# Kernel optimization log

Measured on AMD Instinct MI355X. Metric: run time of the kernel, lower is better.

Reference implementation:

```python
import jax, jax.numpy as jnp
import numpy as np

D_MODEL = 1024
HEADS = 16
D_K = D_MODEL // HEADS


def setup_inputs() -> dict:
    key = jax.random.key(0)
    ks = jax.random.split(key, 11)
    B, S = 4, 2048
    scale = 1.0 / np.sqrt(D_MODEL)
    return {
        "q": jax.random.normal(ks[0], (B, S, D_MODEL), jnp.float32),
        "k": jax.random.normal(ks[1], (B, S, D_MODEL), jnp.float32),
        "v": jax.random.normal(ks[2], (B, S, D_MODEL), jnp.float32),
        "wq": jax.random.normal(ks[3], (D_MODEL, D_MODEL), jnp.float32) * scale,
        "bq": jax.random.normal(ks[4], (D_MODEL,), jnp.float32) * 0.01,
        "wk": jax.random.normal(ks[5], (D_MODEL, D_MODEL), jnp.float32) * scale,
        "bk": jax.random.normal(ks[6], (D_MODEL,), jnp.float32) * 0.01,
        "wv": jax.random.normal(ks[7], (D_MODEL, D_MODEL), jnp.float32) * scale,
        "bv": jax.random.normal(ks[8], (D_MODEL,), jnp.float32) * 0.01,
        "wo": jax.random.normal(ks[9], (D_MODEL, D_MODEL), jnp.float32) * scale,
        "bo": jax.random.normal(ks[10], (D_MODEL,), jnp.float32) * 0.01,
    }


def reference(q, k, v, wq, bq, wk, bk, wv, bv, wo, bo):
    B, S, _ = q.shape
    # nn.Linear: x @ W^T + b
    qp = q @ wq.T + bq
    kp = k @ wk.T + bk
    vp = v @ wv.T + bv
    # [B, S, D] -> [B, H, S, d_k]
    def split_heads(x):
        return x.reshape(B, S, HEADS, D_K).transpose(0, 2, 1, 3)
    qh, kh, vh = split_heads(qp), split_heads(kp), split_heads(vp)
    # scaled dot-product attention (dropout p=0 -> identity)
    scores = jnp.einsum("bhsd,bhtd->bhst", qh, kh) / jnp.sqrt(jnp.float32(D_K)).astype(qh.dtype)
    attn = jax.nn.softmax(scores, axis=-1)
    ctx = jnp.einsum("bhst,bhtd->bhsd", attn, vh)
    # merge heads and output projection
    ctx = ctx.transpose(0, 2, 1, 3).reshape(B, S, D_MODEL)
    return ctx @ wo.T + bo
```

## Files before the change

### kernel.cpp

```cpp
#include <hip/hip_runtime.h>


typedef __attribute__((ext_vector_type(8))) short bf16x8;
typedef __attribute__((ext_vector_type(4))) float f32x4;
typedef unsigned int u32;

#define DEVI __device__ __forceinline__

static constexpr int S_LEN = 2048;
static constexpr int NH = 16;
static constexpr int DK = 64;
static constexpr float Q_SCALE = 0.125f * 1.44269504088896340736f;

DEVI unsigned short f2b(float f) {
    unsigned int u = __builtin_bit_cast(unsigned int, f);
    u += 0x7fffu + ((u >> 16) & 1u);
    return (unsigned short)(u >> 16);
}

DEVI u32 pkbf16(float a, float b) {
#if __has_builtin(__builtin_amdgcn_cvt_pk_bf16_f32)
    auto r = __builtin_amdgcn_cvt_pk_bf16_f32(a, b);
    return __builtin_bit_cast(u32, r);
#else
    return (u32)f2b(a) | ((u32)f2b(b) << 16);
#endif
}

DEVI float fexp2(float x) {
#if __has_builtin(__builtin_amdgcn_exp2f)
    return __builtin_amdgcn_exp2f(x);
#else
    return exp2f(x);
#endif
}

DEVI f32x4 mfma16(bf16x8 a, bf16x8 b, f32x4 c) {
    return __builtin_amdgcn_mfma_f32_16x16x32_bf16(a, b, c, 0, 0, 0);
}

#define GLL16(g, l)                                                        \
    __builtin_amdgcn_global_load_lds(                                      \
        (const __attribute__((address_space(1))) u32*)(g),                 \
        (__attribute__((address_space(3))) u32*)(l), 16, 0, 0)

__global__ __launch_bounds__(256) void cvt3(
    const float* __restrict__ q, const float* __restrict__ k,
    const float* __restrict__ v, unsigned short* __restrict__ dq,
    unsigned short* __restrict__ dk, unsigned short* __restrict__ dv) {
    const int z = blockIdx.y;
    const float* src = z == 0 ? q : z == 1 ? k : v;
    unsigned short* dst = z == 0 ? dq : z == 1 ? dk : dv;
    long i = ((long)blockIdx.x * 256 + threadIdx.x) * 8;
    float4 v0 = *(const float4*)(src + i);
    float4 v1 = *(const float4*)(src + i + 4);
    uint4 o;
    o.x = pkbf16(v0.x, v0.y);
    o.y = pkbf16(v0.z, v0.w);
    o.z = pkbf16(v1.x, v1.y);
    o.w = pkbf16(v1.z, v1.w);
    *(uint4*)(dst + i) = o;
}

__global__ __launch_bounds__(256) void cvt_w(
    const float* __restrict__ a, const float* __restrict__ b,
    const float* __restrict__ c, const float* __restrict__ d,
    unsigned short* __restrict__ o) {
    const float* src = blockIdx.y == 0 ? a : blockIdx.y == 1 ? b
                     : blockIdx.y == 2 ? c : d;
    unsigned short* dst = o + (long)blockIdx.y * 1048576;
    long i = ((long)blockIdx.x * 256 + threadIdx.x) * 8;
    float4 v0 = *(const float4*)(src + i);
    float4 v1 = *(const float4*)(src + i + 4);
    uint4 ov;
    ov.x = pkbf16(v0.x, v0.y);
    ov.y = pkbf16(v0.z, v0.w);
    ov.z = pkbf16(v1.x, v1.y);
    ov.w = pkbf16(v1.z, v1.w);
    *(uint4*)(dst + i) = ov;
}

__global__ __launch_bounds__(256) void gemm_qkv(
    const unsigned short* __restrict__ aq, const unsigned short* __restrict__ ak,
    const unsigned short* __restrict__ av, const unsigned short* __restrict__ wqkv,
    const float* __restrict__ bq, const float* __restrict__ bk,
    const float* __restrict__ bv, unsigned short* __restrict__ qh,
    unsigned short* __restrict__ kh, unsigned short* __restrict__ vht) {
    __shared__ __align__(16) unsigned short As[2][128 * 32];
    __shared__ __align__(16) unsigned short Bs[2][128 * 32];
    const int tid = threadIdx.x;
    const int w = tid >> 6, l = tid & 63, l16 = l & 15, quad = l >> 4;
    const int wm = (w >> 1) * 64, wn = (w & 1) * 64;
    const int m0 = blockIdx.y * 128, n0 = blockIdx.x * 128;
    const int z = blockIdx.z;
    const unsigned short* A = z == 0 ? aq : z == 1 ? ak : av;
    const unsigned short* W = wqkv + (long)z * 1048576;
    const float* bias = z == 0 ? bq : z == 1 ? bk : bv;

    f32x4 acc[4][4] = {};

    auto stage = [&](int kt, int buf) {
        #pragma unroll
        for (int h = 0; h < 2; ++h) {
            int sb = h * 256 + w * 64;
            int slot = sb + l;
            int row = slot >> 2, c = (slot & 3) ^ ((row >> 1) & 3);
            GLL16(A + (long)(m0 + row) * 1024 + kt + c * 8, &As[buf][sb * 8]);
            GLL16(W + (long)(n0 + row) * 1024 + kt + c * 8, &Bs[buf][sb * 8]);
        }
    };

    stage(0, 0);
    __syncthreads();

    for (int ki = 0; ki < 32; ++ki) {
        if (ki < 31) stage((ki + 1) * 32, (ki + 1) & 1);
        const unsigned short* as = As[ki & 1];
        const unsigned short* bs = Bs[ki & 1];
        bf16x8 a[4], b[4];
        #pragma unroll
        for (int i = 0; i < 4; ++i) {
            int r = wm + i * 16 + l16;
            a[i] = *(const bf16x8*)(as + (r * 4 + (quad ^ ((r >> 1) & 3))) * 8);
        }
        #pragma unroll
        for (int j = 0; j < 4; ++j) {
            int r = wn + j * 16 + l16;
            b[j] = *(const bf16x8*)(bs + (r * 4 + (quad ^ ((r >> 1) & 3))) * 8);
        }
        #pragma unroll
        for (int i = 0; i < 4; ++i)
            #pragma unroll
            for (int j = 0; j < 4; ++j)
                acc[i][j] = mfma16(a[i], b[j], acc[i][j]);
        __syncthreads();
    }

    if (z < 2) {
        unsigned short* out = z == 0 ? qh : kh;
        const float scale = z == 0 ? Q_SCALE : 1.0f;
        #pragma unroll
        for (int j = 0; j < 4; ++j) {
            int n = n0 + wn + j * 16 + l16;
            float bvl = bias[n];
            int hh = n >> 6, dd = n & 63;
            #pragma unroll
            for (int i = 0; i < 4; ++i)
                #pragma unroll
                for (int r = 0; r < 4; ++r) {
                    int m = m0 + wm + i * 16 + quad * 4 + r;
                    int bb = m >> 11, ss = m & 2047;
                    out[(((long)(bb * NH + hh) * S_LEN + ss) * DK) + dd] =
                        f2b((acc[i][j][r] + bvl) * scale);
                }
        }
    } else {
        unsigned short* out = vht;
        #pragma unroll
        for (int j = 0; j < 4; ++j) {
            int n = n0 + wn + j * 16 + l16;
            float bvl = bias[n];
            int hh = n >> 6, dd = n & 63;
            #pragma unroll
            for (int i = 0; i < 4; ++i) {
                int m = m0 + wm + i * 16 + quad * 4;
                int bb = m >> 11, ss = m & 2047;
                uint2 pk;
                pk.x = pkbf16(acc[i][j][0] + bvl, acc[i][j][1] + bvl);
                pk.y = pkbf16(acc[i][j][2] + bvl, acc[i][j][3] + bvl);
                *(uint2*)(out + ((long)(bb * NH + hh) * DK + dd) * S_LEN + ss) = pk;
            }
        }
    }
}

__global__ __launch_bounds__(256) void gemm_out(
    const unsigned short* __restrict__ A, const unsigned short* __restrict__ W,
    const float* __restrict__ bias, float* __restrict__ out) {
    __shared__ __align__(16) unsigned short As[2][128 * 32];
    __shared__ __align__(16) unsigned short Bs[2][128 * 32];
    const int tid = threadIdx.x;
    const int w = tid >> 6, l = tid & 63, l16 = l & 15, quad = l >> 4;
    const int wm = (w >> 1) * 64, wn = (w & 1) * 64;
    const int m0 = blockIdx.y * 128, n0 = blockIdx.x * 128;

    f32x4 acc[4][4] = {};

    auto stage = [&](int kt, int buf) {
        #pragma unroll
        for (int h = 0; h < 2; ++h) {
            int sb = h * 256 + w * 64;
            int slot = sb + l;
            int row = slot >> 2, c = (slot & 3) ^ ((row >> 1) & 3);
            GLL16(A + (long)(m0 + row) * 1024 + kt + c * 8, &As[buf][sb * 8]);
            GLL16(W + (long)(n0 + row) * 1024 + kt + c * 8, &Bs[buf][sb * 8]);
        }
    };

    stage(0, 0);
    __syncthreads();

    for (int ki = 0; ki < 32; ++ki) {
        if (ki < 31) stage((ki + 1) * 32, (ki + 1) & 1);
        const unsigned short* as = As[ki & 1];
        const unsigned short* bs = Bs[ki & 1];
        bf16x8 a[4], b[4];
        #pragma unroll
        for (int i = 0; i < 4; ++i) {
            int r = wm + i * 16 + l16;
            a[i] = *(const bf16x8*)(as + (r * 4 + (quad ^ ((r >> 1) & 3))) * 8);
        }
        #pragma unroll
        for (int j = 0; j < 4; ++j) {
            int r = wn + j * 16 + l16;
            b[j] = *(const bf16x8*)(bs + (r * 4 + (quad ^ ((r >> 1) & 3))) * 8);
        }
        #pragma unroll
        for (int i = 0; i < 4; ++i)
            #pragma unroll
            for (int j = 0; j < 4; ++j)
                acc[i][j] = mfma16(a[i], b[j], acc[i][j]);
        __syncthreads();
    }

    #pragma unroll
    for (int j = 0; j < 4; ++j) {
        int n = n0 + wn + j * 16 + l16;
        float bv = bias[n];
        #pragma unroll
        for (int i = 0; i < 4; ++i)
            #pragma unroll
            for (int r = 0; r < 4; ++r) {
                int m = m0 + wm + i * 16 + quad * 4 + r;
                out[(long)m * 1024 + n] = acc[i][j][r] + bv;
            }
    }
}

__global__ __launch_bounds__(256, 3) void attn(
    const unsigned short* __restrict__ qh, const unsigned short* __restrict__ kh,
    const unsigned short* __restrict__ vht, unsigned short* __restrict__ ctx) {
    __shared__ __align__(16) unsigned short Kb[2][4096];
    __shared__ __align__(16) unsigned short Vb[3][4096];
    __shared__ __align__(16) unsigned short P[128 * 44];

    const int id = blockIdx.y * 16 + blockIdx.x;
    const int id2 = (id & 7) * 128 + (id >> 3);
    const int qt = id2 & 15, bh = id2 >> 4;
    const int tid = threadIdx.x;
    const int w = tid >> 6, l = tid & 63, l16 = l & 15, quad = l >> 4;

    const unsigned short* kh_b = kh + (long)bh * 2048 * 64;
    const unsigned short* vh_b = vht + (long)bh * 64 * 2048;

    const unsigned short* qsrc = qh + ((long)bh * 2048 + qt * 128) * 64;
    bf16x8 qf[2][2];
    #pragma unroll
    for (int dd = 0; dd < 2; ++dd)
        #pragma unroll
        for (int i = 0; i < 2; ++i)
            qf[dd][i] = *(const bf16x8*)(qsrc + (w * 32 + i * 16 + l16) * 64 +
                                         dd * 32 + quad * 8);
    #pragma unroll
    for (int dd = 0; dd < 2; ++dd)
        #pragma unroll
        for (int i = 0; i < 2; ++i)
            asm volatile("" :: "v"(qf[dd][i]));

    auto stage_k = [&](const unsigned short* base, int buf) {
        #pragma unroll
        for (int rr = 0; rr < 2; ++rr) {
            int sb = rr * 256 + w * 64;
            int slot = sb + l;
            int row = slot >> 3, cc = (slot & 7) ^ (row & 7);
            GLL16(base + (long)row * 64 + cc * 8, &Kb[buf][sb * 8]);
        }
    };
    auto stage_v = [&](const unsigned short* vbase, int buf) {
        #pragma unroll
        for (int rr = 0; rr < 2; ++rr) {
            int sb = rr * 256 + w * 64;
            int slot = sb + l;
            int d = slot >> 3, cc = (slot & 7) ^ (d & 7);
            GLL16(vbase + (long)d * 2048 + cc * 8, &Vb[buf][sb * 8]);
        }
    };

    stage_k(kh_b, 0);
    stage_v(vh_b, 0);
    stage_v(vh_b + 64, 1);
    asm volatile("s_waitcnt vmcnt(2)" ::: "memory");
    __builtin_amdgcn_s_barrier();
    __builtin_amdgcn_sched_barrier(0);

    f32x4 o[4][2] = {};
    f32x4 osum[2] = {};
    bf16x8 ones;
    #pragma unroll
    for (int j = 0; j < 8; ++j) ones[j] = (short)0x3f80;

    const unsigned short* kstage = kh_b + 64 * 64;
    const unsigned short* vstage = vh_b + 2 * 64;
    int vr = 0, vs = 2;
    for (int kt = 0; kt < 32; ++kt) {
        if (kt < 31) stage_k(kstage, (kt + 1) & 1);
        if (kt < 30) stage_v(vstage, vs);
        kstage += 64 * 64;
        vstage += 64;
        __builtin_amdgcn_sched_barrier(0);

        const unsigned short* kb = Kb[kt & 1];
        f32x4 sa[2][4] = {};
        #pragma unroll
        for (int dd = 0; dd < 2; ++dd) {
            bf16x8 kf[4];
            #pragma unroll
            for (int ja = 0; ja < 4; ++ja) {
                int row = ja * 16 + l16;
                kf[ja] = *(const bf16x8*)(kb + (row * 8 + ((dd * 4 + quad) ^ (row & 7))) * 8);
            }
            __builtin_amdgcn_s_setprio(1);
            #pragma unroll
            for (int i = 0; i < 2; ++i)
                #pragma unroll
                for (int ja = 0; ja < 4; ++ja)
                    sa[i][ja] = mfma16(kf[ja], qf[dd][i], sa[i][ja]);
            __builtin_amdgcn_s_setprio(0);
        }

        #pragma unroll
        for (int i = 0; i < 2; ++i)
            #pragma unroll
            for (int ja = 0; ja < 4; ++ja)
                #pragma unroll
                for (int r = 0; r < 4; ++r)
                    sa[i][ja][r] = fexp2(sa[i][ja][r]);

        const unsigned short* vb = Vb[vr];
        #pragma unroll
        for (int qtr = 0; qtr < 2; ++qtr) {
            #pragma unroll
            for (int jh = 0; jh < 2; ++jh)
                #pragma unroll
                for (int i = 0; i < 2; ++i) {
                    int row = w * 32 + i * 16 + l16;
                    int ja = qtr * 2 + jh;
                    uint2 pk;
                    pk.x = pkbf16(sa[i][ja][0], sa[i][ja][1]);
                    pk.y = pkbf16(sa[i][ja][2], sa[i][ja][3]);
                    *(uint2*)(&P[row * 44 + jh * 16 + quad * 4]) = pk;
                }
            bf16x8 vf[4], pf[2];
            #pragma unroll
            for (int jd = 0; jd < 4; ++jd) {
                int d = jd * 16 + l16;
                vf[jd] = *(const bf16x8*)(vb + (d * 8 + ((qtr * 4 + quad) ^ (d & 7))) * 8);
            }
            #pragma unroll
            for (int i = 0; i < 2; ++i) {
                int row = w * 32 + i * 16 + l16;
                pf[i] = *(const bf16x8*)(&P[row * 44 + quad * 8]);
            }
            __builtin_amdgcn_s_setprio(1);
            #pragma unroll
            for (int jd = 0; jd < 4; ++jd)
                #pragma unroll
                for (int i = 0; i < 2; ++i)
                    o[jd][i] = mfma16(vf[jd], pf[i], o[jd][i]);
            #pragma unroll
            for (int i = 0; i < 2; ++i)
                osum[i] = mfma16(ones, pf[i], osum[i]);
            __builtin_amdgcn_s_setprio(0);
        }

        if (kt < 30) {
            asm volatile("s_waitcnt vmcnt(2)" ::: "memory");
        } else if (kt == 30) {
            asm volatile("s_waitcnt vmcnt(0)" ::: "memory");
        }
        if (kt < 31) {
            __builtin_amdgcn_s_barrier();
            __builtin_amdgcn_sched_barrier(0);
        }

        vr = (vr + 1 == 3) ? 0 : vr + 1;
        vs = (vs + 1 == 3) ? 0 : vs + 1;
    }

    const int b = bh >> 4, hh = bh & 15;
    #pragma unroll
    for (int i = 0; i < 2; ++i) {
        float inv = 1.0f / osum[i][0];
        int s = qt * 128 + w * 32 + i * 16 + l16;
        #pragma unroll
        for (int jd = 0; jd < 4; ++jd) {
            uint2 pk;
            pk.x = pkbf16(o[jd][i][0] * inv, o[jd][i][1] * inv);
            pk.y = pkbf16(o[jd][i][2] * inv, o[jd][i][3] * inv);
            *(uint2*)(&ctx[((long)(b * 2048 + s) * 1024) + hh * 64 + jd * 16 + quad * 4]) = pk;
        }
    }
}

extern "C" void kernel_launch(void* const* d_in, const int* in_sizes, int n_in,
                              void* d_out, int out_size, void* d_ws, size_t ws_size,
                              hipStream_t stream) {
    const float* q  = (const float*)d_in[0];
    const float* k  = (const float*)d_in[1];
    const float* v  = (const float*)d_in[2];
    const float* wq = (const float*)d_in[3];
    const float* bq = (const float*)d_in[4];
    const float* wk = (const float*)d_in[5];
    const float* bk = (const float*)d_in[6];
    const float* wv = (const float*)d_in[7];
    const float* bv = (const float*)d_in[8];
    const float* wo = (const float*)d_in[9];
    const float* bo = (const float*)d_in[10];
    float* out = (float*)d_out;

    const size_t NE = 8u * 1024u * 1024u;
    unsigned short* ab_q = (unsigned short*)d_ws;
    unsigned short* qh   = ab_q + NE;
    unsigned short* kh   = qh + NE;
    unsigned short* vht  = kh + NE;
    unsigned short* wb   = vht + NE;
    unsigned short* wob  = wb + 3 * 1048576;
    unsigned short* ctx  = ab_q;
    unsigned short* ab_k = (unsigned short*)d_out;
    unsigned short* ab_v = ab_k + NE;

    dim3 blk(256);
    cvt_w<<<dim3(512, 4), blk, 0, stream>>>(wq, wk, wv, wo, wb);
    cvt3<<<dim3(4096, 3), blk, 0, stream>>>(q, k, v, ab_q, ab_k, ab_v);
    gemm_qkv<<<dim3(8, 64, 3), blk, 0, stream>>>(ab_q, ab_k, ab_v, wb,
                                                 bq, bk, bv, qh, kh, vht);
    attn<<<dim3(16, 64), blk, 0, stream>>>(qh, kh, vht, ctx);
    gemm_out<<<dim3(8, 64), blk, 0, stream>>>(ctx, wob, bo, out);
}
```

Baseline: 372.8 us.

## Software-pipeline QK^T of next tile with softmax/PV of previous tile

Restructures the attention loop so each step computes the QK^T scores for tile t+1 while doing exp, P packing and the PV MFMAs for tile t. This uses two score register sets and a third K buffer, with manual unrolling by two. The aim is to overlap the exp/VALU work with MFMA work and hide LDS latency. The extra live registers force launch bounds down from 3 to 2 waves per SIMD, so occupancy drops, and the extra K buffer uses more LDS.

```diff
diff --git a/kernel.cpp b/kernel.cpp
--- a/kernel.cpp
+++ b/kernel.cpp
@@ -237,10 +237,10 @@
     }
 }
 
-__global__ __launch_bounds__(256, 3) void attn(
+__global__ __launch_bounds__(256, 2) void attn(
     const unsigned short* __restrict__ qh, const unsigned short* __restrict__ kh,
     const unsigned short* __restrict__ vht, unsigned short* __restrict__ ctx) {
-    __shared__ __align__(16) unsigned short Kb[2][4096];
+    __shared__ __align__(16) unsigned short Kb[3][4096];
     __shared__ __align__(16) unsigned short Vb[3][4096];
     __shared__ __align__(16) unsigned short P[128 * 44];
 
@@ -266,6 +266,7 @@
         #pragma unroll
         for (int i = 0; i < 2; ++i)
             asm volatile("" :: "v"(qf[dd][i]));
+    __builtin_amdgcn_sched_barrier(0);
 
     auto stage_k = [&](const unsigned short* base, int buf) {
         #pragma unroll
@@ -286,31 +287,20 @@
         }
     };
 
-    stage_k(kh_b, 0);
-    stage_v(vh_b, 0);
-    stage_v(vh_b + 64, 1);
-    asm volatile("s_waitcnt vmcnt(2)" ::: "memory");
-    __builtin_amdgcn_s_barrier();
-    __builtin_amdgcn_sched_barrier(0);
-
     f32x4 o[4][2] = {};
     f32x4 osum[2] = {};
     bf16x8 ones;
     #pragma unroll
     for (int j = 0; j < 8; ++j) ones[j] = (short)0x3f80;
 
-    const unsigned short* kstage = kh_b + 64 * 64;
-    const unsigned short* vstage = vh_b + 2 * 64;
-    int vr = 0, vs = 2;
-    for (int kt = 0; kt < 32; ++kt) {
-        if (kt < 31) stage_k(kstage, (kt + 1) & 1);
-        if (kt < 30) stage_v(vstage, vs);
-        kstage += 64 * 64;
-        vstage += 64;
-        __builtin_amdgcn_sched_barrier(0);
-
-        const unsigned short* kb = Kb[kt & 1];
-        f32x4 sa[2][4] = {};
+    f32x4 sA[2][4], sB[2][4];
+
+    auto qkt = [&](const unsigned short* kb, f32x4 (&sa)[2][4]) {
+        #pragma unroll
+        for (int i = 0; i < 2; ++i)
+            #pragma unroll
+            for (int ja = 0; ja < 4; ++ja)
+                sa[i][ja] = f32x4{0.f, 0.f, 0.f, 0.f};
         #pragma unroll
         for (int dd = 0; dd < 2; ++dd) {
             bf16x8 kf[4];
@@ -327,7 +317,9 @@
                     sa[i][ja] = mfma16(kf[ja], qf[dd][i], sa[i][ja]);
             __builtin_amdgcn_s_setprio(0);
         }
-
+    };
+
+    auto fin = [&](f32x4 (&sa)[2][4], const unsigned short* vb) {
         #pragma unroll
         for (int i = 0; i < 2; ++i)
             #pragma unroll
@@ -335,8 +327,6 @@
                 #pragma unroll
                 for (int r = 0; r < 4; ++r)
                     sa[i][ja][r] = fexp2(sa[i][ja][r]);
-
-        const unsigned short* vb = Vb[vr];
         #pragma unroll
         for (int qtr = 0; qtr < 2; ++qtr) {
             #pragma unroll
@@ -372,20 +362,50 @@
                 osum[i] = mfma16(ones, pf[i], osum[i]);
             __builtin_amdgcn_s_setprio(0);
         }
-
-        if (kt < 30) {
-            asm volatile("s_waitcnt vmcnt(2)" ::: "memory");
-        } else if (kt == 30) {
-            asm volatile("s_waitcnt vmcnt(0)" ::: "memory");
-        }
-        if (kt < 31) {
-            __builtin_amdgcn_s_barrier();
-            __builtin_amdgcn_sched_barrier(0);
-        }
-
-        vr = (vr + 1 == 3) ? 0 : vr + 1;
-        vs = (vs + 1 == 3) ? 0 : vs + 1;
-    }
+    };
+
+    stage_k(kh_b, 0);
+    stage_v(vh_b, 0);
+    stage_k(kh_b + 4096, 1);
+    stage_v(vh_b + 64, 1);
+    stage_k(kh_b + 8192, 2);
+    asm volatile("s_waitcnt vmcnt(0)" ::: "memory");
+    __builtin_amdgcn_s_barrier();
+    __builtin_amdgcn_sched_barrier(0);
+    qkt(Kb[0], sA);
+    __builtin_amdgcn_s_barrier();
+    __builtin_amdgcn_sched_barrier(0);
+
+    const unsigned short* kstage = kh_b + 3 * 4096;
+    const unsigned short* vstage = vh_b + 2 * 64;
+    int kr = 1, kst = 0, vp = 0, vst = 2;
+
+#define ATTN_STEP(CUR, PRV, DO_K, DO_V, VMC)                               \
+    {                                                                      \
+        if (DO_K) stage_k(kstage, kst);                                    \
+        if (DO_V) stage_v(vstage, vst);                                    \
+        kstage += 4096; vstage += 64;                                      \
+        __builtin_amdgcn_sched_barrier(0);                                 \
+        qkt(Kb[kr], CUR);                                                  \
+        fin(PRV, Vb[vp]);                                                  \
+        asm volatile("s_waitcnt vmcnt(" #VMC ")" ::: "memory");            \
+        __builtin_amdgcn_s_barrier();                                      \
+        __builtin_amdgcn_sched_barrier(0);                                 \
+        kr = kr == 2 ? 0 : kr + 1;                                         \
+        kst = kst == 2 ? 0 : kst + 1;                                      \
+        vp = vp == 2 ? 0 : vp + 1;                                         \
+        vst = vst == 2 ? 0 : vst + 1;                                      \
+    }
+
+    for (int t = 0; t < 14; ++t) {
+        ATTN_STEP(sB, sA, 1, 1, 4)
+        ATTN_STEP(sA, sB, 1, 1, 4)
+    }
+    ATTN_STEP(sB, sA, 1, 1, 4)
+    ATTN_STEP(sA, sB, 0, 1, 2)
+    ATTN_STEP(sB, sA, 0, 0, 0)
+#undef ATTN_STEP
+    fin(sB, Vb[vp]);
 
     const int b = bh >> 4, hh = bh & 15;
     #pragma unroll
```

Result: no change. 379.8 us (+1.9%).

## Use 256x256 tile GEMM core with 8 waves and interleaved prefetch scheduling

Applied to the files above, without the earlier changes.

Replaces the 128x128, K=32 double-buffered GEMM in both projection kernels with a shared 256x256 tile, K=64 core run by 512 threads. The core interleaves global-to-LDS staging with MFMA phases, using sched barriers, explicit vmcnt waits and s_setprio to overlap loads with compute. The aim is more operand reuse per LDS byte and better latency hiding. In exchange it uses 128 KB of LDS per block and launches fewer blocks (384 for QKV, 128 for the output projection), so load balance across CUs gets worse.

```diff
diff --git a/kernel.cpp b/kernel.cpp
--- a/kernel.cpp
+++ b/kernel.cpp
@@ -43,6 +43,9 @@
     __builtin_amdgcn_global_load_lds(                                      \
         (const __attribute__((address_space(1))) u32*)(g),                 \
         (__attribute__((address_space(3))) u32*)(l), 16, 0, 0)
+
+#define SBAR __builtin_amdgcn_sched_barrier(0)
+#define PHB  SBAR; __builtin_amdgcn_s_barrier(); SBAR
 
 __global__ __launch_bounds__(256) void cvt3(
     const float* __restrict__ q, const float* __restrict__ k,
@@ -80,159 +83,179 @@
     *(uint4*)(dst + i) = ov;
 }
 
-__global__ __launch_bounds__(256) void gemm_qkv(
+#define MM8(MH, NH, BB)                                                    \
+    __builtin_amdgcn_s_setprio(1);                                         \
+    _Pragma("unroll") for (int mi = 0; mi < 4; ++mi)                       \
+        _Pragma("unroll") for (int ni = 0; ni < 2; ++ni)                   \
+            _Pragma("unroll") for (int kk = 0; kk < 2; ++kk)               \
+                acc[(MH)*4 + mi][(NH)*2 + ni] = mfma16(                    \
+                    a[mi][kk], BB[ni][kk], acc[(MH)*4 + mi][(NH)*2 + ni]); \
+    __builtin_amdgcn_s_setprio(0);
+
+DEVI void gemm256_core(const unsigned short* __restrict__ Am,
+                       const unsigned short* __restrict__ Wm,
+                       int m0, int n0, int tid, f32x4 (&acc)[8][4]) {
+    __shared__ __align__(16) unsigned short As[2][256 * 64];
+    __shared__ __align__(16) unsigned short Bs[2][256 * 64];
+    const int wid = tid >> 6, l = tid & 63, l16 = l & 15, quad = l >> 4;
+    const int swz = l16 & 7;
+    const int wm = (wid >> 2) * 128, wn = (wid & 3) * 64;
+    unsigned short *As0 = &As[0][0], *As1 = &As[1][0];
+    unsigned short *Bs0 = &Bs[0][0], *Bs1 = &Bs[1][0];
+
+    bf16x8 a[4][2], b0[2][2], b1[2][2];
+
+    auto stg = [&](const unsigned short* Mat, int r0, int ko,
+                   unsigned short* lds, int type) {
+        #pragma unroll
+        for (int pass = 0; pass < 2; ++pass) {
+            int wlr = pass * 64 + wid * 8;
+            int row0 = type == 0 ? (wlr < 64 ? wlr : wlr + 64)
+                     : type == 1 ? 64 + (wlr < 64 ? wlr : wlr + 64)
+                     : type == 2 ? (wlr & 31) + (wlr >> 5) * 64
+                                 : 32 + (wlr & 31) + (wlr >> 5) * 64;
+            int row = row0 + (l >> 3);
+            int cl = (l & 7) ^ (l >> 3);
+            GLL16(Mat + (long)(r0 + row) * 1024 + ko + cl * 8, lds + row0 * 64);
+        }
+    };
+    auto lda = [&](const unsigned short* as, int mh) {
+        #pragma unroll
+        for (int mi = 0; mi < 4; ++mi)
+            #pragma unroll
+            for (int kk = 0; kk < 2; ++kk)
+                a[mi][kk] = *(const bf16x8*)(as +
+                    (wm + (mh * 4 + mi) * 16 + l16) * 64 +
+                    (((kk * 4 + quad) ^ swz) << 3));
+    };
+    auto ldb = [&](const unsigned short* bs, int nh, bf16x8 (&bb)[2][2]) {
+        #pragma unroll
+        for (int ni = 0; ni < 2; ++ni)
+            #pragma unroll
+            for (int kk = 0; kk < 2; ++kk)
+                bb[ni][kk] = *(const bf16x8*)(bs +
+                    (wn + (nh * 2 + ni) * 16 + l16) * 64 +
+                    (((kk * 4 + quad) ^ swz) << 3));
+    };
+
+    stg(Am, m0, 0, As0, 0); stg(Wm, n0, 0, Bs0, 2);
+    stg(Wm, n0, 0, Bs0, 3); stg(Am, m0, 0, As0, 1);
+    stg(Am, m0, 64, As1, 0); stg(Wm, n0, 64, Bs1, 2); stg(Wm, n0, 64, Bs1, 3);
+    asm volatile("s_waitcnt vmcnt(6)" ::: "memory");
+    __builtin_amdgcn_s_barrier(); SBAR;
+
+    #pragma unroll 1
+    for (int it = 0; it < 8; ++it) {
+        const bool F = it < 7;
+        const int ko1 = it * 128 + 64, ko2 = it * 128 + 128, ko3 = it * 128 + 192;
+        lda(As0, 0); ldb(Bs0, 0, b0);
+        stg(Am, m0, ko1, As1, 1);
+        PHB; MM8(0, 0, b0); PHB;
+        ldb(Bs0, 1, b1);
+        if (F) stg(Am, m0, ko2, As0, 0);
+        PHB; MM8(0, 1, b1); PHB;
+        lda(As0, 1);
+        if (F) stg(Wm, n0, ko2, Bs0, 2);
+        PHB; MM8(1, 0, b0); PHB;
+        if (F) stg(Wm, n0, ko2, Bs0, 3);
+        PHB; MM8(1, 1, b1);
+        SBAR;
+        if (F) { asm volatile("s_waitcnt vmcnt(6)" ::: "memory"); }
+        else   { asm volatile("s_waitcnt vmcnt(0)" ::: "memory"); }
+        __builtin_amdgcn_s_barrier(); SBAR;
+        lda(As1, 0); ldb(Bs1, 0, b0);
+        if (F) stg(Am, m0, ko2, As0, 1);
+        PHB; MM8(0, 0, b0); PHB;
+        ldb(Bs1, 1, b1);
+        if (F) stg(Am, m0, ko3, As1, 0);
+        PHB; MM8(0, 1, b1); PHB;
+        lda(As1, 1);
+        if (F) stg(Wm, n0, ko3, Bs1, 2);
+        PHB; MM8(1, 0, b0); PHB;
+        if (F) stg(Wm, n0, ko3, Bs1, 3);
+        PHB; MM8(1, 1, b1);
+        SBAR;
+        if (F) { asm volatile("s_waitcnt vmcnt(6)" ::: "memory"); }
+        __builtin_amdgcn_s_barrier(); SBAR;
+    }
+}
+
+__global__ __launch_bounds__(512, 2) void gemm_qkv(
     const unsigned short* __restrict__ aq, const unsigned short* __restrict__ ak,
     const unsigned short* __restrict__ av, const unsigned short* __restrict__ wqkv,
     const float* __restrict__ bq, const float* __restrict__ bk,
     const float* __restrict__ bv, unsigned short* __restrict__ qh,
     unsigned short* __restrict__ kh, unsigned short* __restrict__ vht) {
-    __shared__ __align__(16) unsigned short As[2][128 * 32];
-    __shared__ __align__(16) unsigned short Bs[2][128 * 32];
     const int tid = threadIdx.x;
-    const int w = tid >> 6, l = tid & 63, l16 = l & 15, quad = l >> 4;
-    const int wm = (w >> 1) * 64, wn = (w & 1) * 64;
-    const int m0 = blockIdx.y * 128, n0 = blockIdx.x * 128;
+    const int wid = tid >> 6, l = tid & 63, l16 = l & 15, quad = l >> 4;
+    const int wm = (wid >> 2) * 128, wn = (wid & 3) * 64;
+    const int m0 = blockIdx.y * 256, n0 = blockIdx.x * 256;
     const int z = blockIdx.z;
-    const unsigned short* A = z == 0 ? aq : z == 1 ? ak : av;
-    const unsigned short* W = wqkv + (long)z * 1048576;
+    const unsigned short* Am = z == 0 ? aq : z == 1 ? ak : av;
+    const unsigned short* Wm = wqkv + (long)z * 1048576;
     const float* bias = z == 0 ? bq : z == 1 ? bk : bv;
 
-    f32x4 acc[4][4] = {};
-
-    auto stage = [&](int kt, int buf) {
-        #pragma unroll
-        for (int h = 0; h < 2; ++h) {
-            int sb = h * 256 + w * 64;
-            int slot = sb + l;
-            int row = slot >> 2, c = (slot & 3) ^ ((row >> 1) & 3);
-            GLL16(A + (long)(m0 + row) * 1024 + kt + c * 8, &As[buf][sb * 8]);
-            GLL16(W + (long)(n0 + row) * 1024 + kt + c * 8, &Bs[buf][sb * 8]);
-        }
-    };
-
-    stage(0, 0);
-    __syncthreads();
-
-    for (int ki = 0; ki < 32; ++ki) {
-        if (ki < 31) stage((ki + 1) * 32, (ki + 1) & 1);
-        const unsigned short* as = As[ki & 1];
-        const unsigned short* bs = Bs[ki & 1];
-        bf16x8 a[4], b[4];
-        #pragma unroll
-        for (int i = 0; i < 4; ++i) {
-            int r = wm + i * 16 + l16;
-            a[i] = *(const bf16x8*)(as + (r * 4 + (quad ^ ((r >> 1) & 3))) * 8);
-        }
-        #pragma unroll
-        for (int j = 0; j < 4; ++j) {
-            int r = wn + j * 16 + l16;
-            b[j] = *(const bf16x8*)(bs + (r * 4 + (quad ^ ((r >> 1) & 3))) * 8);
-        }
-        #pragma unroll
-        for (int i = 0; i < 4; ++i)
-            #pragma unroll
-            for (int j = 0; j < 4; ++j)
-                acc[i][j] = mfma16(a[i], b[j], acc[i][j]);
-        __syncthreads();
-    }
+    f32x4 acc[8][4] = {};
+    gemm256_core(Am, Wm, m0, n0, tid, acc);
 
     if (z < 2) {
         unsigned short* out = z == 0 ? qh : kh;
         const float scale = z == 0 ? Q_SCALE : 1.0f;
         #pragma unroll
-        for (int j = 0; j < 4; ++j) {
-            int n = n0 + wn + j * 16 + l16;
+        for (int ni = 0; ni < 4; ++ni) {
+            int n = n0 + wn + ni * 16 + l16;
             float bvl = bias[n];
             int hh = n >> 6, dd = n & 63;
             #pragma unroll
-            for (int i = 0; i < 4; ++i)
+            for (int mi = 0; mi < 8; ++mi)
                 #pragma unroll
                 for (int r = 0; r < 4; ++r) {
-                    int m = m0 + wm + i * 16 + quad * 4 + r;
+                    int m = m0 + wm + mi * 16 + quad * 4 + r;
                     int bb = m >> 11, ss = m & 2047;
                     out[(((long)(bb * NH + hh) * S_LEN + ss) * DK) + dd] =
-                        f2b((acc[i][j][r] + bvl) * scale);
+                        f2b((acc[mi][ni][r] + bvl) * scale);
                 }
         }
     } else {
-        unsigned short* out = vht;
-        #pragma unroll
-        for (int j = 0; j < 4; ++j) {
-            int n = n0 + wn + j * 16 + l16;
+        #pragma unroll
+        for (int ni = 0; ni < 4; ++ni) {
+            int n = n0 + wn + ni * 16 + l16;
             float bvl = bias[n];
             int hh = n >> 6, dd = n & 63;
             #pragma unroll
-            for (int i = 0; i < 4; ++i) {
-                int m = m0 + wm + i * 16 + quad * 4;
+            for (int mi = 0; mi < 8; ++mi) {
+                int m = m0 + wm + mi * 16 + quad * 4;
                 int bb = m >> 11, ss = m & 2047;
                 uint2 pk;
-                pk.x = pkbf16(acc[i][j][0] + bvl, acc[i][j][1] + bvl);
-                pk.y = pkbf16(acc[i][j][2] + bvl, acc[i][j][3] + bvl);
-                *(uint2*)(out + ((long)(bb * NH + hh) * DK + dd) * S_LEN + ss) = pk;
+                pk.x = pkbf16(acc[mi][ni][0] + bvl, acc[mi][ni][1] + bvl);
+                pk.y = pkbf16(acc[mi][ni][2] + bvl, acc[mi][ni][3] + bvl);
+                *(uint2*)(vht + ((long)(bb * NH + hh) * DK + dd) * S_LEN + ss) = pk;
             }
         }
     }
 }
 
-__global__ __launch_bounds__(256) void gemm_out(
+__global__ __launch_bounds__(512, 2) void gemm_out(
     const unsigned short* __restrict__ A, const unsigned short* __restrict__ W,
     const float* __restrict__ bias, float* __restrict__ out) {
-    __shared__ __align__(16) unsigned short As[2][128 * 32];
-    __shared__ __align__(16) unsigned short Bs[2][128 * 32];
     const int tid = threadIdx.x;
-    const int w = tid >> 6, l = tid & 63, l16 = l & 15, quad = l >> 4;
-    const int wm = (w >> 1) * 64, wn = (w & 1) * 64;
-    const int m0 = blockIdx.y * 128, n0 = blockIdx.x * 128;
-
-    f32x4 acc[4][4] = {};
-
-    auto stage = [&](int kt, int buf) {
-        #pragma unroll
-        for (int h = 0; h < 2; ++h) {
-            int sb = h * 256 + w * 64;
-            int slot = sb + l;
-            int row = slot >> 2, c = (slot & 3) ^ ((row >> 1) & 3);
-            GLL16(A + (long)(m0 + row) * 1024 + kt + c * 8, &As[buf][sb * 8]);
-            GLL16(W + (long)(n0 + row) * 1024 + kt + c * 8, &Bs[buf][sb * 8]);
-        }
-    };
-
-    stage(0, 0);
-    __syncthreads();
-
-    for (int ki = 0; ki < 32; ++ki) {
-        if (ki < 31) stage((ki + 1) * 32, (ki + 1) & 1);
-        const unsigned short* as = As[ki & 1];
-        const unsigned short* bs = Bs[ki & 1];
-        bf16x8 a[4], b[4];
-        #pragma unroll
-        for (int i = 0; i < 4; ++i) {
-            int r = wm + i * 16 + l16;
-            a[i] = *(const bf16x8*)(as + (r * 4 + (quad ^ ((r >> 1) & 3))) * 8);
-        }
-        #pragma unroll
-        for (int j = 0; j < 4; ++j) {
-            int r = wn + j * 16 + l16;
-            b[j] = *(const bf16x8*)(bs + (r * 4 + (quad ^ ((r >> 1) & 3))) * 8);
-        }
-        #pragma unroll
-        for (int i = 0; i < 4; ++i)
-            #pragma unroll
-            for (int j = 0; j < 4; ++j)
-                acc[i][j] = mfma16(a[i], b[j], acc[i][j]);
-        __syncthreads();
-    }
+    const int wid = tid >> 6, l = tid & 63, l16 = l & 15, quad = l >> 4;
+    const int wm = (wid >> 2) * 128, wn = (wid & 3) * 64;
+    const int m0 = blockIdx.y * 256, n0 = blockIdx.x * 256;
+
+    f32x4 acc[8][4] = {};
+    gemm256_core(A, W, m0, n0, tid, acc);
 
     #pragma unroll
-    for (int j = 0; j < 4; ++j) {
-        int n = n0 + wn + j * 16 + l16;
+    for (int ni = 0; ni < 4; ++ni) {
+        int n = n0 + wn + ni * 16 + l16;
         float bv = bias[n];
         #pragma unroll
-        for (int i = 0; i < 4; ++i)
+        for (int mi = 0; mi < 8; ++mi)
             #pragma unroll
             for (int r = 0; r < 4; ++r) {
-                int m = m0 + wm + i * 16 + quad * 4 + r;
-                out[(long)m * 1024 + n] = acc[i][j][r] + bv;
+                int m = m0 + wm + mi * 16 + quad * 4 + r;
+                out[(long)m * 1024 + n] = acc[mi][ni][r] + bv;
             }
     }
 }
@@ -429,11 +452,10 @@
     unsigned short* ab_k = (unsigned short*)d_out;
     unsigned short* ab_v = ab_k + NE;
 
-    dim3 blk(256);
-    cvt_w<<<dim3(512, 4), blk, 0, stream>>>(wq, wk, wv, wo, wb);
-    cvt3<<<dim3(4096, 3), blk, 0, stream>>>(q, k, v, ab_q, ab_k, ab_v);
-    gemm_qkv<<<dim3(8, 64, 3), blk, 0, stream>>>(ab_q, ab_k, ab_v, wb,
-                                                 bq, bk, bv, qh, kh, vht);
-    attn<<<dim3(16, 64), blk, 0, stream>>>(qh, kh, vht, ctx);
-    gemm_out<<<dim3(8, 64), blk, 0, stream>>>(ctx, wob, bo, out);
-}
+    cvt_w<<<dim3(512, 4), dim3(256), 0, stream>>>(wq, wk, wv, wo, wb);
+    cvt3<<<dim3(4096, 3), dim3(256), 0, stream>>>(q, k, v, ab_q, ab_k, ab_v);
+    gemm_qkv<<<dim3(4, 32, 3), dim3(512), 0, stream>>>(ab_q, ab_k, ab_v, wb,
+                                                       bq, bk, bv, qh, kh, vht);
+    attn<<<dim3(16, 64), dim3(256), 0, stream>>>(qh, kh, vht, ctx);
+    gemm_out<<<dim3(4, 32), dim3(512), 0, stream>>>(ctx, wob, bo, out);
+}
```

After: 365.5 us. 2.0% less time.
